# Kernel optimization log

Measured on AMD Instinct MI355X. Metric: run time of the kernel, lower is better.

## Reference

```python
import jax, jax.numpy as jnp
import numpy as np
from jax.ops import segment_sum

N_NODES = 100000
N_EDGES = 1600000
HIDDEN = 128


def gcn_conv(x, src, dst, w, W, b, num_nodes):
    """PyG GCNConv: add self-loops (weight 1), symmetric deg^-1/2 normalization,
    gather from src, scatter-add to dst. x: [N, Fin], W: [Fin, Fout]."""
    loop = jnp.arange(num_nodes, dtype=src.dtype)
    s = jnp.concatenate([src, loop])
    d = jnp.concatenate([dst, loop])
    ww = jnp.concatenate([w, jnp.ones((num_nodes,), dtype=w.dtype)])
    deg = segment_sum(ww, d, num_segments=num_nodes)           # [N]
    dis = jnp.where(deg > 0, jax.lax.rsqrt(jnp.where(deg > 0, deg, 1.0)), 0.0)
    norm = dis[s] * ww * dis[d]                                # [E+N]
    h = x @ W                                                  # [N, Fout]
    msg = norm[:, None] * h[s]                                 # [E+N, Fout]
    out = segment_sum(msg, d, num_segments=num_nodes)          # [N, Fout]
    return out + b


def setup_inputs() -> dict:
    key = jax.random.key(0)
    ks = jax.random.split(key, 12)
    h = HIDDEN
    sc = lambda fan_in: 1.0 / np.sqrt(fan_in)
    return {
        "x": jax.random.normal(ks[0], (N_NODES, 1), dtype=jnp.float32),
        "edge_index": jax.random.randint(ks[1], (2, N_EDGES), 0, N_NODES, dtype=jnp.int64),
        "edge_weight": jax.random.uniform(ks[2], (N_EDGES,), dtype=jnp.float32),
        "W1": jax.random.normal(ks[3], (1, h), dtype=jnp.float32) * sc(1),
        "b1": jnp.zeros((h,), dtype=jnp.float32),
        "W2": jax.random.normal(ks[4], (h, 2 * h), dtype=jnp.float32) * sc(h),
        "b2": jnp.zeros((2 * h,), dtype=jnp.float32),
        "Wl1": jax.random.normal(ks[5], (2 * h, h), dtype=jnp.float32) * sc(2 * h),
        "bl1": jnp.zeros((h,), dtype=jnp.float32),
        "Wl2": jax.random.normal(ks[6], (h, 1), dtype=jnp.float32) * sc(h),
        "bl2": jnp.zeros((1,), dtype=jnp.float32),
    }


def reference(x, edge_index, edge_weight, W1, b1, W2, b2, Wl1, bl1, Wl2, bl2):
    n = x.shape[0]
    src, dst = edge_index[0], edge_index[1]
    h = jax.nn.relu(gcn_conv(x, src, dst, edge_weight, W1, b1, n))
    h = jax.nn.relu(gcn_conv(h, src, dst, edge_weight, W2, b2, n))
    h = jax.nn.relu(h @ Wl1 + bl1)
    return h @ Wl2 + bl2
```

## Files before the change

### kernel.cpp

```cpp
#include <hip/hip_runtime.h>


#define HD 128
#define HD2 256
#define BSHIFT 8
#define BNODES 256
#define SRCBITS 17

typedef __attribute__((ext_vector_type(8))) short bf8_t;
typedef __attribute__((ext_vector_type(4))) float f32x4;

static inline size_t align256(size_t x) { return (x + 255) & ~(size_t)255; }

__device__ inline ushort f2bf(float f) {
    uint u = __float_as_uint(f);
    uint r = u + 0x7fffu + ((u >> 16) & 1u);
    return (ushort)(r >> 16);
}
__device__ inline uint packbf(float a, float b) {
    return (uint)f2bf(a) | ((uint)f2bf(b) << 16);
}

__global__ __launch_bounds__(256) void k_part(const int* __restrict__ ei,
                                              const float* __restrict__ ew,
                                              int* __restrict__ bfill,
                                              uint2* __restrict__ stg,
                                              int E, int nbuck, int cap) {
    __shared__ int lcnt[512];
    __shared__ int lbase[512];
    int tid = threadIdx.x;
    for (int i = tid; i < nbuck; i += 256) lcnt[i] = 0;
    __syncthreads();
    bool is64 = (ei[1] == 0) && (ei[3] == 0) && (ei[5] == 0) && (ei[7] == 0);
    int e0 = blockIdx.x * 2048;
    uint pack[8]; uint wb[8]; int bkt[8]; int rank[8];
    for (int u = 0; u < 8; u++) {
        int e = e0 + u * 256 + tid;
        bkt[u] = -1;
        if (e < E) {
            int s, d;
            if (is64) { s = ei[2 * e]; d = ei[2 * (E + e)]; }
            else      { s = ei[e];     d = ei[E + e]; }
            bkt[u] = d >> BSHIFT;
            pack[u] = ((uint)(d & (BNODES - 1)) << SRCBITS) | (uint)s;
            wb[u] = __float_as_uint(ew[e]);
            rank[u] = atomicAdd(&lcnt[bkt[u]], 1);
        }
    }
    __syncthreads();
    for (int i = tid; i < nbuck; i += 256)
        lbase[i] = lcnt[i] ? atomicAdd(&bfill[i], lcnt[i]) : 0;
    __syncthreads();
    for (int u = 0; u < 8; u++)
        if (bkt[u] >= 0)
            stg[(size_t)bkt[u] * cap + lbase[bkt[u]] + rank[u]] =
                make_uint2(pack[u], wb[u]);
}

__global__ __launch_bounds__(512) void k_bscan(const int* __restrict__ bfill,
                                               int* __restrict__ cvbase,
                                               int* __restrict__ rowptr,
                                               int nbuck, int N, int E) {
    __shared__ int ws[8];
    int tid = threadIdx.x;
    int lane = tid & 63, wvid = tid >> 6;
    int a = (tid < nbuck) ? bfill[tid] : 0;
    int v = a;
    for (int off = 1; off < 64; off <<= 1) {
        int u = __shfl_up(v, off);
        if (lane >= off) v += u;
    }
    if (lane == 63) ws[wvid] = v;
    __syncthreads();
    int wpre = 0;
    for (int k = 0; k < wvid; k++) wpre += ws[k];
    if (tid < nbuck) cvbase[tid] = v + wpre - a;
    if (tid == 0) rowptr[N] = E;
}

__global__ __launch_bounds__(512) void k_fine(const uint2* __restrict__ stg,
                                              const int* __restrict__ bfill,
                                              const int* __restrict__ cvbase,
                                              const float* __restrict__ x,
                                              float* __restrict__ dis,
                                              float* __restrict__ p,
                                              int* __restrict__ rowptr,
                                              int2* __restrict__ cv,
                                              int cap, int N) {
    __shared__ int cnt_l[BNODES];
    __shared__ int base_l[BNODES];
    __shared__ float degf[BNODES];
    __shared__ int wsum[4];
    int b = blockIdx.x, tid = threadIdx.x;
    int n = bfill[b];
    int cb = cvbase[b];
    const uint2* s = stg + (size_t)b * cap;
    if (tid < BNODES) { cnt_l[tid] = 0; degf[tid] = 1.0f; }
    __syncthreads();
    for (int i = tid; i < n; i += 512)
        atomicAdd(&cnt_l[s[i].x >> SRCBITS], 1);
    __syncthreads();
    int lane = tid & 63, wvid = tid >> 6;
    int a = 0;
    if (tid < BNODES) { a = cnt_l[tid]; cnt_l[tid] = 0; }
    int v = a;
    for (int off = 1; off < 64; off <<= 1) {
        int u = __shfl_up(v, off);
        if (lane >= off) v += u;
    }
    if (wvid < 4 && lane == 63) wsum[wvid] = v;
    __syncthreads();
    if (tid < BNODES) {
        int wpre = 0;
        for (int k = 0; k < wvid; k++) wpre += wsum[k];
        base_l[tid] = v + wpre - a;
    }
    __syncthreads();
    for (int i = tid; i < n; i += 512) {
        uint2 r = s[i];
        int dl = r.x >> SRCBITS;
        int src = (int)(r.x & ((1u << SRCBITS) - 1));
        int pos = cb + base_l[dl] + atomicAdd(&cnt_l[dl], 1);
        cv[pos] = make_int2(src, (int)r.y);
        atomicAdd(&degf[dl], __uint_as_float(r.y));
    }
    __syncthreads();
    int gid = (b << BSHIFT) + tid;
    if (tid < BNODES && gid < N) {
        rowptr[gid] = cb + base_l[tid];
        float r = rsqrtf(degf[tid]);
        dis[gid] = r;
        p[gid] = r * x[gid];
    }
}

__global__ void k_prepB(const float* __restrict__ W2, const float* __restrict__ Wl1,
                        ushort* __restrict__ Bt1, ushort* __restrict__ Bt2) {
    int o = blockIdx.x * blockDim.x + threadIdx.x;
    if (o >= 32768) return;
    {
        int k0 = o & 7, n = (o >> 3) & 255, k8 = o >> 11;
        Bt1[o] = f2bf(W2[(size_t)(k8 * 8 + k0) * 256 + n]);
    }
    {
        int k0 = o & 7, n = (o >> 3) & 127, k8 = o >> 10;
        Bt2[o] = f2bf(Wl1[(size_t)(k8 * 8 + k0) * 128 + n]);
    }
}

__global__ __launch_bounds__(256) void k_q(const int* __restrict__ rowptr,
                                           const int2* __restrict__ cv,
                                           const float* __restrict__ dis,
                                           const float* __restrict__ p,
                                           float2* __restrict__ tp, int N) {
    int gid = blockIdx.x * blockDim.x + threadIdx.x;
    int wid = gid >> 4;
    int sl = threadIdx.x & 15;
    if (wid >= N) return;
    int beg = rowptr[wid], end = rowptr[wid + 1];
    float s = 0.0f;
    for (int i = beg + sl; i < end; i += 16) {
        int2 pr = cv[i];
        s += __int_as_float(pr.y) * p[pr.x];
    }
    s += __shfl_xor(s, 1);
    s += __shfl_xor(s, 2);
    s += __shfl_xor(s, 4);
    s += __shfl_xor(s, 8);
    if (sl == 0) {
        float r = dis[wid];
        tp[wid] = make_float2(r * (s + p[wid]), r);
    }
}

__global__ __launch_bounds__(256) void k_agg(const int* __restrict__ rowptr,
                                             const int2* __restrict__ cv,
                                             const float2* __restrict__ tp,
                                             const float* __restrict__ W1,
                                             const float* __restrict__ b1,
                                             uint* __restrict__ z, int N) {
    __shared__ float4 eb[4][32];
    int tid = threadIdx.x;
    int wvid = tid >> 6, lane = tid & 63;
    int wid = (blockIdx.x * blockDim.x + tid) >> 6;
    if (wid >= N) return;
    float2 w1 = *(const float2*)(W1 + lane * 2);
    float2 bb = *(const float2*)(b1 + lane * 2);
    int beg = rowptr[wid], end = rowptr[wid + 1];
    float ax = 0.0f, ay = 0.0f;
    for (int base = beg; base < end; base += 64) {
        int eidx = base + lane;
        float wd = 0.0f, tt = 0.0f;
        if (eidx < end) {
            int2 pr = cv[eidx];
            float2 tps = tp[pr.x];
            wd = __int_as_float(pr.y) * tps.y;
            tt = tps.x;
        }
        ((float2*)&eb[wvid][0])[lane] = make_float2(wd, tt);
        int m = min(64, end - base);
        const float4* ebp = &eb[wvid][0];
        int halves = (m + 1) >> 1;
        for (int u = 0; u < halves; u++) {
            float4 e2 = ebp[u];
            float f0 = fmaxf(fmaf(e2.y, w1.x, bb.x), 0.0f);
            float f1 = fmaxf(fmaf(e2.y, w1.y, bb.y), 0.0f);
            ax = fmaf(e2.x, f0, ax);
            ay = fmaf(e2.x, f1, ay);
            float g0 = fmaxf(fmaf(e2.w, w1.x, bb.x), 0.0f);
            float g1 = fmaxf(fmaf(e2.w, w1.y, bb.y), 0.0f);
            ax = fmaf(e2.z, g0, ax);
            ay = fmaf(e2.z, g1, ay);
        }
    }
    float2 tpd = tp[wid];
    float rd = tpd.y;
    float s0 = rd * fmaxf(fmaf(tpd.x, w1.x, bb.x), 0.0f);
    float s1 = rd * fmaxf(fmaf(tpd.x, w1.y, bb.y), 0.0f);
    z[(size_t)wid * 64 + lane] = packbf(rd * (ax + s0), rd * (ay + s1));
}

__global__ __launch_bounds__(256) void k_mlp(const ushort* __restrict__ A,
                                             const ushort* __restrict__ Bt1,
                                             const ushort* __restrict__ Bt2,
                                             const float* __restrict__ b2,
                                             const float* __restrict__ bl1,
                                             const float* __restrict__ wl2,
                                             const float* __restrict__ bl2,
                                             float* __restrict__ out, int M) {
    __shared__ ushort st[4][32][40];
    int tid = threadIdx.x;
    int wv = tid >> 6, lane = tid & 63;
    int l15 = lane & 15, quad = lane >> 4;
    int row0 = blockIdx.x * 128 + wv * 32;
    int r0 = row0 + l15;      r0 = r0 < M ? r0 : M - 1;
    int r1 = row0 + 16 + l15; r1 = r1 < M ? r1 : M - 1;

    bf8_t a1[2][4];
    for (int kc = 0; kc < 4; kc++) {
        a1[0][kc] = *(const bf8_t*)(A + (size_t)r0 * 128 + kc * 32 + quad * 8);
        a1[1][kc] = *(const bf8_t*)(A + (size_t)r1 * 128 + kc * 32 + quad * 8);
    }
    f32x4 acc2[2][8];
    for (int i = 0; i < 2; i++)
        for (int j = 0; j < 8; j++) acc2[i][j] = (f32x4){0.f, 0.f, 0.f, 0.f};

    for (int c = 0; c < 8; c++) {
        f32x4 acc1[2][2];
        for (int i = 0; i < 2; i++)
            for (int j = 0; j < 2; j++) acc1[i][j] = (f32x4){0.f, 0.f, 0.f, 0.f};
        for (int kc = 0; kc < 4; kc++)
            for (int nt = 0; nt < 2; nt++) {
                bf8_t b = *(const bf8_t*)(Bt1 +
                    ((size_t)(kc * 4 + quad) * 256 + c * 32 + nt * 16 + l15) * 8);
                acc1[0][nt] = __builtin_amdgcn_mfma_f32_16x16x32_bf16(a1[0][kc], b, acc1[0][nt], 0, 0, 0);
                acc1[1][nt] = __builtin_amdgcn_mfma_f32_16x16x32_bf16(a1[1][kc], b, acc1[1][nt], 0, 0, 0);
            }
        for (int nt = 0; nt < 2; nt++) {
            float bb = b2[c * 32 + nt * 16 + l15];
            for (int mt = 0; mt < 2; mt++)
                for (int rg = 0; rg < 4; rg++)
                    st[wv][mt * 16 + quad * 4 + rg][nt * 16 + l15] =
                        f2bf(fmaxf(acc1[mt][nt][rg] + bb, 0.f));
        }
        bf8_t a2_0 = *(const bf8_t*)&st[wv][l15][quad * 8];
        bf8_t a2_1 = *(const bf8_t*)&st[wv][16 + l15][quad * 8];
        for (int nt2 = 0; nt2 < 8; nt2++) {
            bf8_t b = *(const bf8_t*)(Bt2 +
                ((size_t)(c * 4 + quad) * 128 + nt2 * 16 + l15) * 8);
            acc2[0][nt2] = __builtin_amdgcn_mfma_f32_16x16x32_bf16(a2_0, b, acc2[0][nt2], 0, 0, 0);
            acc2[1][nt2] = __builtin_amdgcn_mfma_f32_16x16x32_bf16(a2_1, b, acc2[1][nt2], 0, 0, 0);
        }
    }
    float rs[2][4] = {};
    for (int nt2 = 0; nt2 < 8; nt2++) {
        int col = nt2 * 16 + l15;
        float bb = bl1[col], ww = wl2[col];
        for (int mt = 0; mt < 2; mt++)
            for (int rg = 0; rg < 4; rg++)
                rs[mt][rg] += fmaxf(acc2[mt][nt2][rg] + bb, 0.f) * ww;
    }
    float base = bl2[0];
    for (int mt = 0; mt < 2; mt++)
        for (int rg = 0; rg < 4; rg++) {
            float s = rs[mt][rg];
            s += __shfl_xor(s, 1);
            s += __shfl_xor(s, 2);
            s += __shfl_xor(s, 4);
            s += __shfl_xor(s, 8);
            int row = row0 + mt * 16 + quad * 4 + rg;
            if (l15 == 0 && row < M) out[row] = s + base;
        }
}

extern "C" void kernel_launch(void* const* d_in, const int* in_sizes, int n_in,
                              void* d_out, int out_size, void* d_ws, size_t ws_size,
                              hipStream_t stream) {
    const float* x   = (const float*)d_in[0];
    const int*   ei  = (const int*)d_in[1];
    const float* ew  = (const float*)d_in[2];
    const float* W1  = (const float*)d_in[3];
    const float* b1  = (const float*)d_in[4];
    const float* W2  = (const float*)d_in[5];
    const float* b2  = (const float*)d_in[6];
    const float* Wl1 = (const float*)d_in[7];
    const float* bl1 = (const float*)d_in[8];
    const float* Wl2 = (const float*)d_in[9];
    const float* bl2 = (const float*)d_in[10];
    float* out = (float*)d_out;
    const int N = in_sizes[0];
    const int E = in_sizes[2];

    const int nbuck = (N + BNODES - 1) >> BSHIFT;
    const int cap = ((E / nbuck) * 5) / 4 + 1024;

    char* w = (char*)d_ws;
    size_t off = 0;
    auto alloc = [&](size_t bytes) -> void* {
        void* p = w + off;
        off = align256(off + bytes);
        return p;
    };
    uint*   z      = (uint*)alloc((size_t)N * 64 * 4);
    float2* tp     = (float2*)alloc((size_t)N * 8);
    float*  dis    = (float*)alloc((size_t)N * 4);
    float*  p_     = (float*)alloc((size_t)N * 4);
    int*    rowptr = (int*)alloc((size_t)(N + 1) * 4);
    int2*   cv     = (int2*)alloc((size_t)E * 8);
    uint2*  stg    = (uint2*)alloc((size_t)nbuck * cap * 8);
    int*    bfill  = (int*)alloc(512 * 4);
    int*    cvbase = (int*)alloc(512 * 4);
    ushort* Bt1    = (ushort*)alloc(32768 * 2);
    ushort* Bt2    = (ushort*)alloc(32768 * 2);

    hipMemsetAsync(bfill, 0, 512 * 4, stream);
    k_part<<<(E + 2047) / 2048, 256, 0, stream>>>(ei, ew, bfill, stg, E, nbuck, cap);
    k_bscan<<<1, 512, 0, stream>>>(bfill, cvbase, rowptr, nbuck, N, E);
    k_fine<<<nbuck, 512, 0, stream>>>(stg, bfill, cvbase, x, dis, p_, rowptr, cv, cap, N);
    k_prepB<<<128, 256, 0, stream>>>(W2, Wl1, Bt1, Bt2);
    k_q<<<(N * 16 + 255) / 256, 256, 0, stream>>>(rowptr, cv, dis, p_, tp, N);
    k_agg<<<(N + 3) / 4, 256, 0, stream>>>(rowptr, cv, tp, W1, b1, z, N);
    k_mlp<<<(N + 127) / 128, 256, 0, stream>>>((const ushort*)z, Bt1, Bt2,
                                               b2, bl1, Wl2, bl2, out, N);
}
```

Measured before the change: 213.0 us.

## Use per-wave bucket counters, split aggregation accumulators, stage MLP weights in LDS

Three unrelated changes. The partition kernel now keeps a separate set of LDS bucket counters for each wave, which cuts contention on the shared-memory atomics, and combines them with a prefix when reserving global slots. The aggregation loop is unrolled by two and uses two independent accumulator pairs to shorten the FMA dependency chain. The MLP kernel loads each chunk's B1 and B2 weight tiles into LDS cooperatively instead of having every wave read them from global memory, at the cost of two block barriers per chunk and extra LDS use.

Measured after the change: 219.9 us. +3.2%, slower.

```diff
diff --git a/kernel.cpp b/kernel.cpp
--- a/kernel.cpp
+++ b/kernel.cpp
@@ -26,10 +26,13 @@
                                               int* __restrict__ bfill,
                                               uint2* __restrict__ stg,
                                               int E, int nbuck, int cap) {
-    __shared__ int lcnt[512];
-    __shared__ int lbase[512];
+    __shared__ int lcnt[4][512];
+    __shared__ int lbase[4][512];
     int tid = threadIdx.x;
-    for (int i = tid; i < nbuck; i += 256) lcnt[i] = 0;
+    int wvid = tid >> 6;
+    for (int i = tid; i < nbuck; i += 256) {
+        lcnt[0][i] = 0; lcnt[1][i] = 0; lcnt[2][i] = 0; lcnt[3][i] = 0;
+    }
     __syncthreads();
     bool is64 = (ei[1] == 0) && (ei[3] == 0) && (ei[5] == 0) && (ei[7] == 0);
     int e0 = blockIdx.x * 2048;
@@ -44,16 +47,23 @@
             bkt[u] = d >> BSHIFT;
             pack[u] = ((uint)(d & (BNODES - 1)) << SRCBITS) | (uint)s;
             wb[u] = __float_as_uint(ew[e]);
-            rank[u] = atomicAdd(&lcnt[bkt[u]], 1);
-        }
-    }
-    __syncthreads();
-    for (int i = tid; i < nbuck; i += 256)
-        lbase[i] = lcnt[i] ? atomicAdd(&bfill[i], lcnt[i]) : 0;
+            rank[u] = atomicAdd(&lcnt[wvid][bkt[u]], 1);
+        }
+    }
+    __syncthreads();
+    for (int i = tid; i < nbuck; i += 256) {
+        int t0 = lcnt[0][i], t1 = lcnt[1][i], t2 = lcnt[2][i], t3 = lcnt[3][i];
+        int tot = t0 + t1 + t2 + t3;
+        int base = tot ? atomicAdd(&bfill[i], tot) : 0;
+        lbase[0][i] = base;
+        lbase[1][i] = base + t0;
+        lbase[2][i] = base + t0 + t1;
+        lbase[3][i] = base + t0 + t1 + t2;
+    }
     __syncthreads();
     for (int u = 0; u < 8; u++)
         if (bkt[u] >= 0)
-            stg[(size_t)bkt[u] * cap + lbase[bkt[u]] + rank[u]] =
+            stg[(size_t)bkt[u] * cap + lbase[wvid][bkt[u]] + rank[u]] =
                 make_uint2(pack[u], wb[u]);
 }
 
@@ -187,7 +197,7 @@
     float2 w1 = *(const float2*)(W1 + lane * 2);
     float2 bb = *(const float2*)(b1 + lane * 2);
     int beg = rowptr[wid], end = rowptr[wid + 1];
-    float ax = 0.0f, ay = 0.0f;
+    float ax0 = 0.0f, ay0 = 0.0f, ax1 = 0.0f, ay1 = 0.0f;
     for (int base = beg; base < end; base += 64) {
         int eidx = base + lane;
         float wd = 0.0f, tt = 0.0f;
@@ -201,18 +211,28 @@
         int m = min(64, end - base);
         const float4* ebp = &eb[wvid][0];
         int halves = (m + 1) >> 1;
-        for (int u = 0; u < halves; u++) {
+        int u = 0;
+        for (; u + 2 <= halves; u += 2) {
             float4 e2 = ebp[u];
-            float f0 = fmaxf(fmaf(e2.y, w1.x, bb.x), 0.0f);
-            float f1 = fmaxf(fmaf(e2.y, w1.y, bb.y), 0.0f);
-            ax = fmaf(e2.x, f0, ax);
-            ay = fmaf(e2.x, f1, ay);
-            float g0 = fmaxf(fmaf(e2.w, w1.x, bb.x), 0.0f);
-            float g1 = fmaxf(fmaf(e2.w, w1.y, bb.y), 0.0f);
-            ax = fmaf(e2.z, g0, ax);
-            ay = fmaf(e2.z, g1, ay);
-        }
-    }
+            float4 e3 = ebp[u + 1];
+            ax0 = fmaf(e2.x, fmaxf(fmaf(e2.y, w1.x, bb.x), 0.0f), ax0);
+            ay0 = fmaf(e2.x, fmaxf(fmaf(e2.y, w1.y, bb.y), 0.0f), ay0);
+            ax1 = fmaf(e2.z, fmaxf(fmaf(e2.w, w1.x, bb.x), 0.0f), ax1);
+            ay1 = fmaf(e2.z, fmaxf(fmaf(e2.w, w1.y, bb.y), 0.0f), ay1);
+            ax0 = fmaf(e3.x, fmaxf(fmaf(e3.y, w1.x, bb.x), 0.0f), ax0);
+            ay0 = fmaf(e3.x, fmaxf(fmaf(e3.y, w1.y, bb.y), 0.0f), ay0);
+            ax1 = fmaf(e3.z, fmaxf(fmaf(e3.w, w1.x, bb.x), 0.0f), ax1);
+            ay1 = fmaf(e3.z, fmaxf(fmaf(e3.w, w1.y, bb.y), 0.0f), ay1);
+        }
+        if (u < halves) {
+            float4 e2 = ebp[u];
+            ax0 = fmaf(e2.x, fmaxf(fmaf(e2.y, w1.x, bb.x), 0.0f), ax0);
+            ay0 = fmaf(e2.x, fmaxf(fmaf(e2.y, w1.y, bb.y), 0.0f), ay0);
+            ax1 = fmaf(e2.z, fmaxf(fmaf(e2.w, w1.x, bb.x), 0.0f), ax1);
+            ay1 = fmaf(e2.z, fmaxf(fmaf(e2.w, w1.y, bb.y), 0.0f), ay1);
+        }
+    }
+    float ax = ax0 + ax1, ay = ay0 + ay1;
     float2 tpd = tp[wid];
     float rd = tpd.y;
     float s0 = rd * fmaxf(fmaf(tpd.x, w1.x, bb.x), 0.0f);
@@ -228,6 +248,8 @@
                                              const float* __restrict__ wl2,
                                              const float* __restrict__ bl2,
                                              float* __restrict__ out, int M) {
+    __shared__ ushort sB1[4096];
+    __shared__ ushort sB2[4096];
     __shared__ ushort st[4][32][40];
     int tid = threadIdx.x;
     int wv = tid >> 6, lane = tid & 63;
@@ -246,39 +268,51 @@
         for (int j = 0; j < 8; j++) acc2[i][j] = (f32x4){0.f, 0.f, 0.f, 0.f};
 
     for (int c = 0; c < 8; c++) {
+        {
+            uint4* s1 = (uint4*)sB1;
+            for (int i = tid; i < 512; i += 256) {
+                int r = i >> 5, j = i & 31;
+                s1[i] = ((const uint4*)(Bt1 + ((size_t)(r * 256 + c * 32)) * 8))[j];
+            }
+            uint4* s2 = (uint4*)sB2;
+            const uint4* g2 = (const uint4*)(Bt2 + (size_t)c * 4096);
+            for (int i = tid; i < 512; i += 256) s2[i] = g2[i];
+        }
+        __syncthreads();
         f32x4 acc1[2][2];
         for (int i = 0; i < 2; i++)
             for (int j = 0; j < 2; j++) acc1[i][j] = (f32x4){0.f, 0.f, 0.f, 0.f};
         for (int kc = 0; kc < 4; kc++)
             for (int nt = 0; nt < 2; nt++) {
-                bf8_t b = *(const bf8_t*)(Bt1 +
-                    ((size_t)(kc * 4 + quad) * 256 + c * 32 + nt * 16 + l15) * 8);
+                bf8_t b = *(const bf8_t*)(sB1 +
+                    ((size_t)((kc * 4 + quad) * 32 + nt * 16 + l15)) * 8);
                 acc1[0][nt] = __builtin_amdgcn_mfma_f32_16x16x32_bf16(a1[0][kc], b, acc1[0][nt], 0, 0, 0);
                 acc1[1][nt] = __builtin_amdgcn_mfma_f32_16x16x32_bf16(a1[1][kc], b, acc1[1][nt], 0, 0, 0);
             }
         for (int nt = 0; nt < 2; nt++) {
-            float bb = b2[c * 32 + nt * 16 + l15];
+            float bbv = b2[c * 32 + nt * 16 + l15];
             for (int mt = 0; mt < 2; mt++)
                 for (int rg = 0; rg < 4; rg++)
                     st[wv][mt * 16 + quad * 4 + rg][nt * 16 + l15] =
-                        f2bf(fmaxf(acc1[mt][nt][rg] + bb, 0.f));
+                        f2bf(fmaxf(acc1[mt][nt][rg] + bbv, 0.f));
         }
         bf8_t a2_0 = *(const bf8_t*)&st[wv][l15][quad * 8];
         bf8_t a2_1 = *(const bf8_t*)&st[wv][16 + l15][quad * 8];
         for (int nt2 = 0; nt2 < 8; nt2++) {
-            bf8_t b = *(const bf8_t*)(Bt2 +
-                ((size_t)(c * 4 + quad) * 128 + nt2 * 16 + l15) * 8);
+            bf8_t b = *(const bf8_t*)(sB2 +
+                ((size_t)(quad * 128 + nt2 * 16 + l15)) * 8);
             acc2[0][nt2] = __builtin_amdgcn_mfma_f32_16x16x32_bf16(a2_0, b, acc2[0][nt2], 0, 0, 0);
             acc2[1][nt2] = __builtin_amdgcn_mfma_f32_16x16x32_bf16(a2_1, b, acc2[1][nt2], 0, 0, 0);
         }
+        __syncthreads();
     }
     float rs[2][4] = {};
     for (int nt2 = 0; nt2 < 8; nt2++) {
         int col = nt2 * 16 + l15;
-        float bb = bl1[col], ww = wl2[col];
+        float bbv = bl1[col], ww = wl2[col];
         for (int mt = 0; mt < 2; mt++)
             for (int rg = 0; rg < 4; rg++)
-                rs[mt][rg] += fmaxf(acc2[mt][nt2][rg] + bb, 0.f) * ww;
+                rs[mt][rg] += fmaxf(acc2[mt][nt2][rg] + bbv, 0.f) * ww;
     }
     float base = bl2[0];
     for (int mt = 0; mt < 2; mt++)
```
